# Kernel optimization log

Hardware: AMD Instinct MI355X
Metric: run time of the kernel (lower is better)

The kernel has to match this reference:

```python
import jax, jax.numpy as jnp
import numpy as np

D_MODEL = 1024
N_HEAD = 16


def setup_inputs() -> dict:
    key = jax.random.key(0)
    ks = jax.random.split(key, 9)
    d = D_MODEL
    s = 0.02
    return {
        "x": jax.random.normal(ks[0], (4, 2048, d), dtype=jnp.float32),
        "w_q": jax.random.normal(ks[1], (d, d), dtype=jnp.float32) * s,
        "b_q": jax.random.normal(ks[2], (d,), dtype=jnp.float32) * s,
        "w_k": jax.random.normal(ks[3], (d, d), dtype=jnp.float32) * s,
        "b_k": jax.random.normal(ks[4], (d,), dtype=jnp.float32) * s,
        "w_v": jax.random.normal(ks[5], (d, d), dtype=jnp.float32) * s,
        "b_v": jax.random.normal(ks[6], (d,), dtype=jnp.float32) * s,
        "w_o": jax.random.normal(ks[7], (d, d), dtype=jnp.float32) * s,
        "b_o": jax.random.normal(ks[8], (d,), dtype=jnp.float32) * s,
    }


def reference(x, w_q, b_q, w_k, b_k, w_v, b_v, w_o, b_o):
    B, S, D = x.shape
    H = N_HEAD
    dh = D // H

    def split(t):  # [B,S,D] -> [B,H,S,dh]
        return t.reshape(B, S, H, dh).transpose(0, 2, 1, 3)

    q = split(x @ w_q + b_q)
    k = split(x @ w_k + b_k)
    v = split(x @ w_v + b_v)

    scale = 1.0 / jnp.sqrt(jnp.float32(dh))
    score = jnp.einsum("bhqd,bhkd->bhqk", q, k) * scale
    score = jax.nn.softmax(score, axis=-1)
    out = jnp.einsum("bhqk,bhkd->bhqd", score, v)
    out = out.transpose(0, 2, 1, 3).reshape(B, S, D)
    return out @ w_o + b_o
```

## Files before the change

### kernel.cpp

```cpp
#include <hip/hip_runtime.h>


typedef __bf16 bf16x8 __attribute__((ext_vector_type(8)));
typedef float f32x4 __attribute__((ext_vector_type(4)));
typedef float f32x16 __attribute__((ext_vector_type(16)));
typedef unsigned short u16x8 __attribute__((ext_vector_type(8)));
typedef unsigned u32x4 __attribute__((ext_vector_type(4)));
typedef unsigned u32x2 __attribute__((ext_vector_type(2)));

#define SEQ 2048
#define DM 1024
#define NHEAD 16
#define MTOT 8192
#define QSCALE 0.18033688011112042f

__device__ __forceinline__ unsigned short f2bf(float f) {
  unsigned u = __builtin_bit_cast(unsigned, f);
  u += 0x7fffu + ((u >> 16) & 1u);
  return (unsigned short)(u >> 16);
}

__device__ __forceinline__ unsigned pkbf(float lo, float hi) {
  __bf16 a = (__bf16)lo, b = (__bf16)hi;
  return ((unsigned)__builtin_bit_cast(unsigned short, b) << 16) |
         __builtin_bit_cast(unsigned short, a);
}

__device__ __forceinline__ void async16(const void* g, void* l) {
  __builtin_amdgcn_global_load_lds(
      (const __attribute__((address_space(1))) void*)g,
      (__attribute__((address_space(3))) void*)l, 16, 0, 0);
}

template <bool CX>
__device__ __forceinline__ void exch(unsigned A, unsigned B, unsigned& fr0, unsigned& fr2) {
#if __has_builtin(__builtin_amdgcn_permlane32_swap)
  if constexpr (CX) {
    u32x2 r = __builtin_amdgcn_permlane32_swap(B, A, false, false);
    fr0 = r[1]; fr2 = r[0];
  } else {
    u32x2 r = __builtin_amdgcn_permlane32_swap(A, B, false, false);
    fr0 = r[0]; fr2 = r[1];
  }
#else
  int hi = (threadIdx.x & 63) >> 5;
  unsigned sA = (unsigned)__shfl_xor((int)A, 32);
  unsigned sB = (unsigned)__shfl_xor((int)B, 32);
  fr0 = hi ? sB : A;
  fr2 = hi ? B : sA;
#endif
}

__device__ __forceinline__ float halfsum(float rs) {
#if __has_builtin(__builtin_amdgcn_permlane32_swap)
  unsigned rb = __builtin_bit_cast(unsigned, rs);
  u32x2 rr = __builtin_amdgcn_permlane32_swap(rb, rb, false, false);
  return __builtin_bit_cast(float, rr[0]) + __builtin_bit_cast(float, rr[1]);
#else
  return rs + __shfl_xor(rs, 32);
#endif
}

__global__ __launch_bounds__(256) void k_cvt(const float* __restrict__ x,
                                             unsigned short* __restrict__ xb) {
  size_t i = ((size_t)blockIdx.x * 256 + threadIdx.x) * 8;
  float4 a = *(const float4*)(x + i);
  float4 b = *(const float4*)(x + i + 4);
  u16x8 o;
  o[0] = f2bf(a.x); o[1] = f2bf(a.y); o[2] = f2bf(a.z); o[3] = f2bf(a.w);
  o[4] = f2bf(b.x); o[5] = f2bf(b.y); o[6] = f2bf(b.z); o[7] = f2bf(b.w);
  *(u16x8*)(xb + i) = o;
}

__global__ __launch_bounds__(256) void k_wt(const float* __restrict__ w0, const float* __restrict__ w1,
                                            const float* __restrict__ w2, const float* __restrict__ w3,
                                            unsigned short* __restrict__ t0, unsigned short* __restrict__ t1,
                                            unsigned short* __restrict__ t2, unsigned short* __restrict__ t3) {
  __shared__ float t[64][65];
  int z = blockIdx.z;
  const float* w = z == 0 ? w0 : z == 1 ? w1 : z == 2 ? w2 : w3;
  unsigned short* wt = z == 0 ? t0 : z == 1 ? t1 : z == 2 ? t2 : t3;
  int nt = blockIdx.x, kt = blockIdx.y;
  int tx = threadIdx.x & 63, ty = threadIdx.x >> 6;
  for (int i = 0; i < 16; ++i) {
    int r = i * 4 + ty;
    t[r][tx] = w[(size_t)(kt * 64 + r) * DM + nt * 64 + tx];
  }
  __syncthreads();
  for (int i = 0; i < 16; ++i) {
    int r = i * 4 + ty;
    wt[(size_t)(nt * 64 + r) * DM + kt * 64 + tx] = f2bf(t[tx][r]);
  }
}

__device__ __forceinline__ void gemm_body(const unsigned short* __restrict__ A,
                                          const unsigned short* __restrict__ Bt,
                                          const float* __restrict__ bias,
                                          unsigned short* __restrict__ Cb,
                                          float* __restrict__ Cf, int bm, int bn, float sc) {
  __shared__ __align__(16) unsigned short As[128 * 64];
  __shared__ __align__(16) unsigned short Bs[128 * 64];
  const int K = DM, N = DM;
  int tid = threadIdx.x, w = tid >> 6, l = tid & 63;
  int g = l >> 4, l15 = l & 15;
  int wm = (w >> 1) * 64, wn = (w & 1) * 64;
  f32x4 acc[4][4];
#pragma unroll
  for (int mi = 0; mi < 4; ++mi)
#pragma unroll
    for (int ni = 0; ni < 4; ++ni)
#pragma unroll
      for (int e = 0; e < 4; ++e) acc[mi][ni][e] = 0.f;

  int lr8 = l >> 3, lp = l & 7;
  for (int kt = 0; kt < K / 64; ++kt) {
    __syncthreads();
#pragma unroll
    for (int i = 0; i < 4; ++i) {
      int cs = i * 4 + w;
      int row = cs * 8 + lr8;
      int c = lp ^ lr8;
      async16(A + (size_t)(bm + row) * K + kt * 64 + c * 8, &As[cs * 512]);
      async16(Bt + (size_t)(bn + row) * K + kt * 64 + c * 8, &Bs[cs * 512]);
    }
    __syncthreads();
    bf16x8 af[4][2];
#pragma unroll
    for (int mi = 0; mi < 4; ++mi)
#pragma unroll
      for (int kk = 0; kk < 2; ++kk) {
        int row = wm + mi * 16 + l15;
        af[mi][kk] = *(const bf16x8*)&As[row * 64 + (((kk * 4 + g) ^ (row & 7)) * 8)];
      }
    __builtin_amdgcn_s_setprio(1);
#pragma unroll
    for (int ni = 0; ni < 4; ++ni) {
      int row = wn + ni * 16 + l15;
      bf16x8 b0 = *(const bf16x8*)&Bs[row * 64 + (((0 + g) ^ (row & 7)) * 8)];
      bf16x8 b1 = *(const bf16x8*)&Bs[row * 64 + (((4 + g) ^ (row & 7)) * 8)];
#pragma unroll
      for (int mi = 0; mi < 4; ++mi) {
        acc[mi][ni] = __builtin_amdgcn_mfma_f32_16x16x32_bf16(af[mi][0], b0, acc[mi][ni], 0, 0, 0);
        acc[mi][ni] = __builtin_amdgcn_mfma_f32_16x16x32_bf16(af[mi][1], b1, acc[mi][ni], 0, 0, 0);
      }
    }
    __builtin_amdgcn_s_setprio(0);
  }
  float bv[4];
#pragma unroll
  for (int ni = 0; ni < 4; ++ni) bv[ni] = bias[bn + wn + ni * 16 + l15];
#pragma unroll
  for (int mi = 0; mi < 4; ++mi)
#pragma unroll
    for (int ni = 0; ni < 4; ++ni) {
      int col = bn + wn + ni * 16 + l15;
#pragma unroll
      for (int r = 0; r < 4; ++r) {
        int rowg = bm + wm + mi * 16 + g * 4 + r;
        float v = (acc[mi][ni][r] + bv[ni]) * sc;
        if (Cf) Cf[(size_t)rowg * N + col] = v;
        else    Cb[(size_t)rowg * N + col] = f2bf(v);
      }
    }
}

__global__ __launch_bounds__(256) void k_gemm(const unsigned short* __restrict__ A,
                                              const unsigned short* __restrict__ Bt,
                                              const float* __restrict__ bias,
                                              unsigned short* __restrict__ Cb,
                                              float* __restrict__ Cf) {
  gemm_body(A, Bt, bias, Cb, Cf, blockIdx.y * 128, blockIdx.x * 128, 1.f);
}

__global__ __launch_bounds__(256) void k_gemm_qkv(const unsigned short* __restrict__ A,
                                                  const unsigned short* bt0, const unsigned short* bt1,
                                                  const unsigned short* bt2,
                                                  const float* b0, const float* b1, const float* b2,
                                                  unsigned short* o0, unsigned short* o1,
                                                  unsigned short* o2) {
  int which = blockIdx.x >> 3;
  const unsigned short* Bt = which == 0 ? bt0 : which == 1 ? bt1 : bt2;
  const float* bias = which == 0 ? b0 : which == 1 ? b1 : b2;
  unsigned short* Cb = which == 0 ? o0 : which == 1 ? o1 : o2;
  float sc = which == 0 ? QSCALE : 1.f;
  gemm_body(A, Bt, bias, Cb, nullptr, blockIdx.y * 128, (blockIdx.x & 7) * 128, sc);
}

__global__ __launch_bounds__(256) void k_vt(const unsigned short* __restrict__ V,
                                            unsigned short* __restrict__ Vt) {
  __shared__ __align__(16) unsigned short t[64 * 64];
  int st = blockIdx.x, bh = blockIdx.y;
  int b = bh >> 4, h = bh & 15;
  int tid = threadIdx.x, w = tid >> 6, l = tid & 63;
  for (int i = 0; i < 2; ++i) {
    int cs = i * 4 + w;
    int row = cs * 8 + (l >> 3);
    int c = l & 7;
    async16(V + ((size_t)(b * SEQ + st * 64 + row) * DM + h * 64 + c * 8), &t[cs * 512]);
  }
  __syncthreads();
  for (int p = 0; p < 2; ++p) {
    int d = p * 32 + (tid >> 3);
    int cs = tid & 7;
    u16x8 o;
    for (int j = 0; j < 8; ++j) o[j] = t[(cs * 8 + j) * 64 + d];
    *(u16x8*)(Vt + ((size_t)bh * 64 + d) * SEQ + st * 64 + cs * 8) = o;
  }
}

template <bool CX>
__device__ __forceinline__ void attn_core(const unsigned short* __restrict__ Q,
                                          const unsigned short* __restrict__ Kg,
                                          const unsigned short* __restrict__ Vt,
                                          unsigned short* __restrict__ Og,
                                          unsigned short* smem, int b, int h, int bh, int qt) {
  int tid = threadIdx.x, w = tid >> 6, l = tid & 63;
  int l31 = l & 31, hi = l >> 5, l7 = l & 7;
  int lr8 = l >> 3, lp = l & 7;
  int q0w = qt * 256 + w * 64;
  unsigned short* const ks0 = smem;
  unsigned short* const ks1 = smem + 4096;
  unsigned short* const vs0 = smem + 8192;
  unsigned short* const vs1 = smem + 12288;

  bf16x8 qf[2][4];
#pragma unroll
  for (int qh = 0; qh < 2; ++qh)
#pragma unroll
    for (int c = 0; c < 4; ++c)
      qf[qh][c] = *(const bf16x8*)(Q + (size_t)(b * SEQ + q0w + qh * 32 + l31) * DM +
                                   h * 64 + c * 16 + hi * 8);

  float lrow[2] = {0.f, 0.f};
  f32x16 oacc[2][2];
#pragma unroll
  for (int qh = 0; qh < 2; ++qh)
#pragma unroll
    for (int d = 0; d < 2; ++d)
#pragma unroll
      for (int r = 0; r < 16; ++r) oacc[qh][d][r] = 0.f;

  auto stage = [&](int kt, unsigned short* kdst, unsigned short* vdst) {
#pragma unroll
    for (int i = 0; i < 2; ++i) {
      int cs = i * 4 + w;
      int row = cs * 8 + lr8;
      int c = lp ^ lr8;
      async16(Kg + ((size_t)(b * SEQ + kt * 64 + row) * DM + h * 64 + c * 8), kdst + cs * 512);
      async16(Vt + (((size_t)bh * 64 + row) * SEQ + kt * 64 + c * 8), vdst + cs * 512);
    }
  };

  auto tile = [&](int kt, unsigned short* kc, unsigned short* vc,
                  unsigned short* kn, unsigned short* vn) {
    if (kt + 1 < SEQ / 64) stage(kt + 1, kn, vn);

    f32x16 sacc[2][2];
#pragma unroll
    for (int qh = 0; qh < 2; ++qh)
#pragma unroll
      for (int kh = 0; kh < 2; ++kh)
#pragma unroll
        for (int r = 0; r < 16; ++r) sacc[qh][kh][r] = 0.f;
    __builtin_amdgcn_s_setprio(1);
#pragma unroll
    for (int kh = 0; kh < 2; ++kh) {
      const unsigned short* kb = kc + (kh * 32 + l31) * 64;
#pragma unroll
      for (int c = 0; c < 4; ++c) {
        bf16x8 a = *(const bf16x8*)(kb + (((2 * c + hi) ^ l7) << 3));
        sacc[0][kh] = __builtin_amdgcn_mfma_f32_32x32x16_bf16(a, qf[0][c], sacc[0][kh], 0, 0, 0);
        sacc[1][kh] = __builtin_amdgcn_mfma_f32_32x32x16_bf16(a, qf[1][c], sacc[1][kh], 0, 0, 0);
      }
    }
    __builtin_amdgcn_s_setprio(0);

    bf16x8 pf[2][4];
#pragma unroll
    for (int qh = 0; qh < 2; ++qh) {
      float r0 = 0.f, r1 = 0.f, r2 = 0.f, r3 = 0.f;
#pragma unroll
      for (int kh = 0; kh < 2; ++kh)
#pragma unroll
        for (int e = 0; e < 16; e += 4) {
          float p0 = __builtin_amdgcn_exp2f(sacc[qh][kh][e + 0]);
          float p1 = __builtin_amdgcn_exp2f(sacc[qh][kh][e + 1]);
          float p2 = __builtin_amdgcn_exp2f(sacc[qh][kh][e + 2]);
          float p3 = __builtin_amdgcn_exp2f(sacc[qh][kh][e + 3]);
          sacc[qh][kh][e + 0] = p0; sacc[qh][kh][e + 1] = p1;
          sacc[qh][kh][e + 2] = p2; sacc[qh][kh][e + 3] = p3;
          r0 += p0; r1 += p1; r2 += p2; r3 += p3;
        }
      lrow[qh] += halfsum((r0 + r1) + (r2 + r3));
#pragma unroll
      for (int ks = 0; ks < 4; ++ks) {
        int kh = ks >> 1, q4 = (ks & 1) * 8;
        unsigned A0 = pkbf(sacc[qh][kh][q4 + 0], sacc[qh][kh][q4 + 1]);
        unsigned A1 = pkbf(sacc[qh][kh][q4 + 2], sacc[qh][kh][q4 + 3]);
        unsigned B0 = pkbf(sacc[qh][kh][q4 + 4], sacc[qh][kh][q4 + 5]);
        unsigned B1 = pkbf(sacc[qh][kh][q4 + 6], sacc[qh][kh][q4 + 7]);
        unsigned f0, f1, f2, f3;
        exch<CX>(A0, B0, f0, f2);
        exch<CX>(A1, B1, f1, f3);
        u32x4 fr; fr[0] = f0; fr[1] = f1; fr[2] = f2; fr[3] = f3;
        pf[qh][ks] = __builtin_bit_cast(bf16x8, fr);
      }
    }

    __builtin_amdgcn_s_setprio(1);
#pragma unroll
    for (int d = 0; d < 2; ++d) {
      const unsigned short* vb = vc + (d * 32 + l31) * 64;
#pragma unroll
      for (int ks = 0; ks < 4; ++ks) {
        bf16x8 a = *(const bf16x8*)(vb + (((2 * ks + hi) ^ l7) << 3));
        oacc[0][d] = __builtin_amdgcn_mfma_f32_32x32x16_bf16(a, pf[0][ks], oacc[0][d], 0, 0, 0);
        oacc[1][d] = __builtin_amdgcn_mfma_f32_32x32x16_bf16(a, pf[1][ks], oacc[1][d], 0, 0, 0);
      }
    }
    __builtin_amdgcn_s_setprio(0);
    __syncthreads();
  };

  stage(0, ks0, vs0);
  __syncthreads();
  for (int kt = 0; kt < SEQ / 64; kt += 2) {
    tile(kt, ks0, vs0, ks1, vs1);
    tile(kt + 1, ks1, vs1, ks0, vs0);
  }

  unsigned* ot = (unsigned*)smem + w * (32 * 33);
#pragma unroll
  for (int qh = 0; qh < 2; ++qh) {
    float inv = 1.f / lrow[qh];
#pragma unroll
    for (int d = 0; d < 2; ++d)
#pragma unroll
      for (int qd = 0; qd < 4; ++qd) {
        unsigned u0 = pkbf(oacc[qh][d][qd * 4 + 0] * inv, oacc[qh][d][qd * 4 + 1] * inv);
        unsigned u1 = pkbf(oacc[qh][d][qd * 4 + 2] * inv, oacc[qh][d][qd * 4 + 3] * inv);
        int idx = l31 * 33 + d * 16 + qd * 4 + hi * 2;
        ot[idx] = u0;
        ot[idx + 1] = u1;
      }
    int row = l >> 1, half = l & 1;
    const unsigned* sr = (const unsigned*)smem + w * (32 * 33) + row * 33 + half * 16;
    unsigned o[16];
#pragma unroll
    for (int j = 0; j < 16; ++j) o[j] = sr[j];
    size_t gbase = (size_t)(b * SEQ + q0w + qh * 32 + row) * DM + h * 64 + half * 32;
#pragma unroll
    for (int i = 0; i < 4; ++i) {
      u32x4 t;
      t[0] = o[i * 4 + 0]; t[1] = o[i * 4 + 1]; t[2] = o[i * 4 + 2]; t[3] = o[i * 4 + 3];
      *(u32x4*)(Og + gbase * 1 + i * 8) = t;
    }
  }
}

__global__ __launch_bounds__(256, 2) void k_attn(const unsigned short* __restrict__ Q,
                                                 const unsigned short* __restrict__ Kg,
                                                 const unsigned short* __restrict__ Vt,
                                                 unsigned short* __restrict__ Og) {
  __shared__ __align__(16) unsigned short smem[16384];
  int bh = blockIdx.x, qt = blockIdx.y;
  int b = bh >> 4, h = bh & 15;
#if __has_builtin(__builtin_amdgcn_permlane32_swap)
  unsigned lid = threadIdx.x & 63;
  u32x2 pr = __builtin_amdgcn_permlane32_swap(lid, lid + 64u, false, false);
  bool convX = __builtin_amdgcn_readfirstlane(pr[0]) >= 64u;
#else
  bool convX = false;
#endif
  if (convX) attn_core<true>(Q, Kg, Vt, Og, smem, b, h, bh, qt);
  else       attn_core<false>(Q, Kg, Vt, Og, smem, b, h, bh, qt);
}

extern "C" void kernel_launch(void* const* d_in, const int* in_sizes, int n_in,
                              void* d_out, int out_size, void* d_ws, size_t ws_size,
                              hipStream_t stream) {
  const float* x  = (const float*)d_in[0];
  const float* wq = (const float*)d_in[1];
  const float* bq = (const float*)d_in[2];
  const float* wk = (const float*)d_in[3];
  const float* bk = (const float*)d_in[4];
  const float* wv = (const float*)d_in[5];
  const float* bv = (const float*)d_in[6];
  const float* wo = (const float*)d_in[7];
  const float* bo = (const float*)d_in[8];

  const size_t SZ_X = (size_t)MTOT * DM * 2;
  const size_t SZ_W = (size_t)DM * DM * 2;
  char* ws = (char*)d_ws;
  size_t off = 0;
  unsigned short* xb  = (unsigned short*)(ws + off); off += SZ_X;
  unsigned short* wqT = (unsigned short*)(ws + off); off += SZ_W;
  unsigned short* wkT = (unsigned short*)(ws + off); off += SZ_W;
  unsigned short* wvT = (unsigned short*)(ws + off); off += SZ_W;
  unsigned short* woT = (unsigned short*)(ws + off); off += SZ_W;
  unsigned short* Qb  = (unsigned short*)(ws + off); off += SZ_X;
  unsigned short* Kb  = (unsigned short*)(ws + off); off += SZ_X;
  unsigned short* Vb  = (unsigned short*)(ws + off); off += SZ_X;
  unsigned short* Vtb = (unsigned short*)(ws + off); off += SZ_X;
  unsigned short* Ab  = (unsigned short*)(ws + off); off += SZ_X;
  if (ws_size < off) return;

  k_cvt<<<dim3(4096), dim3(256), 0, stream>>>(x, xb);
  k_wt<<<dim3(16, 16, 4), dim3(256), 0, stream>>>(wq, wk, wv, wo, wqT, wkT, wvT, woT);
  k_gemm_qkv<<<dim3(24, 64), dim3(256), 0, stream>>>(xb, wqT, wkT, wvT, bq, bk, bv, Qb, Kb, Vb);
  k_vt<<<dim3(32, 64), dim3(256), 0, stream>>>(Vb, Vtb);
  k_attn<<<dim3(64, 8), dim3(256), 0, stream>>>(Qb, Kb, Vtb, Ab);
  k_gemm<<<dim3(8, 64), dim3(256), 0, stream>>>(Ab, woT, bo, nullptr, (float*)d_out);
}
```

Measured before the change: 181.2 us.

## Deepen attention K/V prefetch to a 4-slot ring with explicit vmcnt waits

The attention kernel moves from a double-buffered K/V stage with a full __syncthreads per tile to a four-slot LDS ring. Loads are issued two tiles ahead and gated by explicit s_waitcnt vmcnt(4) plus a raw s_barrier, which aims to hide global-to-LDS latency and drop the implicit full waitcnt. LDS per block doubles to 64 KB, which may limit occupancy under launch_bounds(256,2). The first QK MFMA now takes a zero accumulator directly instead of zero-initialising sacc.

Measured after the change: 181.9 us. Within noise of the previous version (+0.4%).

```diff
diff --git a/kernel.cpp b/kernel.cpp
--- a/kernel.cpp
+++ b/kernel.cpp
@@ -218,10 +218,8 @@
   int l31 = l & 31, hi = l >> 5, l7 = l & 7;
   int lr8 = l >> 3, lp = l & 7;
   int q0w = qt * 256 + w * 64;
-  unsigned short* const ks0 = smem;
-  unsigned short* const ks1 = smem + 4096;
-  unsigned short* const vs0 = smem + 8192;
-  unsigned short* const vs1 = smem + 12288;
+  unsigned short* const KS = smem;
+  unsigned short* const VS = smem + 16384;
 
   bf16x8 qf[2][4];
 #pragma unroll
@@ -231,43 +229,43 @@
       qf[qh][c] = *(const bf16x8*)(Q + (size_t)(b * SEQ + q0w + qh * 32 + l31) * DM +
                                    h * 64 + c * 16 + hi * 8);
 
+  const f32x16 fz = {0.f, 0.f, 0.f, 0.f, 0.f, 0.f, 0.f, 0.f,
+                     0.f, 0.f, 0.f, 0.f, 0.f, 0.f, 0.f, 0.f};
   float lrow[2] = {0.f, 0.f};
   f32x16 oacc[2][2];
 #pragma unroll
   for (int qh = 0; qh < 2; ++qh)
 #pragma unroll
-    for (int d = 0; d < 2; ++d)
-#pragma unroll
-      for (int r = 0; r < 16; ++r) oacc[qh][d][r] = 0.f;
-
-  auto stage = [&](int kt, unsigned short* kdst, unsigned short* vdst) {
+    for (int d = 0; d < 2; ++d) oacc[qh][d] = fz;
+
+  auto stage = [&](int kt) {
+    int s = kt & 3;
+    unsigned short* kd = KS + s * 4096;
+    unsigned short* vd = VS + s * 4096;
 #pragma unroll
     for (int i = 0; i < 2; ++i) {
       int cs = i * 4 + w;
       int row = cs * 8 + lr8;
       int c = lp ^ lr8;
-      async16(Kg + ((size_t)(b * SEQ + kt * 64 + row) * DM + h * 64 + c * 8), kdst + cs * 512);
-      async16(Vt + (((size_t)bh * 64 + row) * SEQ + kt * 64 + c * 8), vdst + cs * 512);
+      async16(Kg + ((size_t)(b * SEQ + kt * 64 + row) * DM + h * 64 + c * 8), kd + cs * 512);
+      async16(Vt + (((size_t)bh * 64 + row) * SEQ + kt * 64 + c * 8), vd + cs * 512);
     }
   };
 
-  auto tile = [&](int kt, unsigned short* kc, unsigned short* vc,
-                  unsigned short* kn, unsigned short* vn) {
-    if (kt + 1 < SEQ / 64) stage(kt + 1, kn, vn);
+  auto compute = [&](int kt) {
+    const unsigned short* kc = KS + (kt & 3) * 4096;
+    const unsigned short* vc = VS + (kt & 3) * 4096;
 
     f32x16 sacc[2][2];
-#pragma unroll
-    for (int qh = 0; qh < 2; ++qh)
-#pragma unroll
-      for (int kh = 0; kh < 2; ++kh)
-#pragma unroll
-        for (int r = 0; r < 16; ++r) sacc[qh][kh][r] = 0.f;
     __builtin_amdgcn_s_setprio(1);
 #pragma unroll
     for (int kh = 0; kh < 2; ++kh) {
       const unsigned short* kb = kc + (kh * 32 + l31) * 64;
-#pragma unroll
-      for (int c = 0; c < 4; ++c) {
+      bf16x8 a0 = *(const bf16x8*)(kb + ((hi ^ l7) << 3));
+      sacc[0][kh] = __builtin_amdgcn_mfma_f32_32x32x16_bf16(a0, qf[0][0], fz, 0, 0, 0);
+      sacc[1][kh] = __builtin_amdgcn_mfma_f32_32x32x16_bf16(a0, qf[1][0], fz, 0, 0, 0);
+#pragma unroll
+      for (int c = 1; c < 4; ++c) {
         bf16x8 a = *(const bf16x8*)(kb + (((2 * c + hi) ^ l7) << 3));
         sacc[0][kh] = __builtin_amdgcn_mfma_f32_32x32x16_bf16(a, qf[0][c], sacc[0][kh], 0, 0, 0);
         sacc[1][kh] = __builtin_amdgcn_mfma_f32_32x32x16_bf16(a, qf[1][c], sacc[1][kh], 0, 0, 0);
@@ -319,15 +317,34 @@
       }
     }
     __builtin_amdgcn_s_setprio(0);
-    __syncthreads();
   };
 
-  stage(0, ks0, vs0);
-  __syncthreads();
-  for (int kt = 0; kt < SEQ / 64; kt += 2) {
-    tile(kt, ks0, vs0, ks1, vs1);
-    tile(kt + 1, ks1, vs1, ks0, vs0);
-  }
+#define VWAIT4 asm volatile("s_waitcnt vmcnt(4)" ::: "memory")
+#define VWAIT0 asm volatile("s_waitcnt vmcnt(0)" ::: "memory")
+#define BARR                         \
+  __builtin_amdgcn_s_barrier();      \
+  __builtin_amdgcn_sched_barrier(0)
+
+  stage(0);
+  stage(1);
+  VWAIT4;
+  BARR;
+  const int NT = SEQ / 64;
+  for (int kt = 0; kt < NT - 2; ++kt) {
+    stage(kt + 2);
+    compute(kt);
+    VWAIT4;
+    BARR;
+  }
+  compute(NT - 2);
+  VWAIT0;
+  BARR;
+  compute(NT - 1);
+  BARR;
+
+#undef VWAIT4
+#undef VWAIT0
+#undef BARR
 
   unsigned* ot = (unsigned*)smem + w * (32 * 33);
 #pragma unroll
@@ -353,7 +370,7 @@
     for (int i = 0; i < 4; ++i) {
       u32x4 t;
       t[0] = o[i * 4 + 0]; t[1] = o[i * 4 + 1]; t[2] = o[i * 4 + 2]; t[3] = o[i * 4 + 3];
-      *(u32x4*)(Og + gbase * 1 + i * 8) = t;
+      *(u32x4*)(Og + gbase + i * 8) = t;
     }
   }
 }
@@ -362,7 +379,7 @@
                                                  const unsigned short* __restrict__ Kg,
                                                  const unsigned short* __restrict__ Vt,
                                                  unsigned short* __restrict__ Og) {
-  __shared__ __align__(16) unsigned short smem[16384];
+  __shared__ __align__(16) unsigned short smem[32768];
   int bh = blockIdx.x, qt = blockIdx.y;
   int b = bh >> 4, h = bh & 15;
 #if __has_builtin(__builtin_amdgcn_permlane32_swap)
```

## Load K/V fragments directly from global into registers, swizzle GEMM block order

Applied to the files above, without the earlier changes.

The attention kernel no longer stages K and V tiles through shared memory with async copies and barriers. Each wave now loads its own 32-key K and V fragments straight from global memory into registers, double-buffered across chunks, and processes 32 keys per step instead of 64. This drops the per-tile __syncthreads and shrinks LDS to the output transpose buffer, at the cost of each wave redundantly fetching K/V from global/L2 instead of sharing it across the four waves. Separately, both GEMM kernels remap block indices so consecutive blocks are spread across rows, aiming for better cache locality.

New measurement: 221.0 us. 22.0% more time.

```diff
diff --git a/kernel.cpp b/kernel.cpp
--- a/kernel.cpp
+++ b/kernel.cpp
@@ -169,7 +169,10 @@
                                               const float* __restrict__ bias,
                                               unsigned short* __restrict__ Cb,
                                               float* __restrict__ Cf) {
-  gemm_body(A, Bt, bias, Cb, Cf, blockIdx.y * 128, blockIdx.x * 128, 1.f);
+  int L = blockIdx.x + blockIdx.y * 8;
+  int Lp = (L & 7) * 64 + (L >> 3);
+  int bx = Lp & 7, by = Lp >> 3;
+  gemm_body(A, Bt, bias, Cb, Cf, by * 128, bx * 128, 1.f);
 }
 
 __global__ __launch_bounds__(256) void k_gemm_qkv(const unsigned short* __restrict__ A,
@@ -178,12 +181,15 @@
                                                   const float* b0, const float* b1, const float* b2,
                                                   unsigned short* o0, unsigned short* o1,
                                                   unsigned short* o2) {
-  int which = blockIdx.x >> 3;
+  int L = blockIdx.x + blockIdx.y * 24;
+  int Lp = (L & 7) * 192 + (L >> 3);
+  int bx = Lp % 24, by = Lp / 24;
+  int which = bx >> 3;
   const unsigned short* Bt = which == 0 ? bt0 : which == 1 ? bt1 : bt2;
   const float* bias = which == 0 ? b0 : which == 1 ? b1 : b2;
   unsigned short* Cb = which == 0 ? o0 : which == 1 ? o1 : o2;
   float sc = which == 0 ? QSCALE : 1.f;
-  gemm_body(A, Bt, bias, Cb, nullptr, blockIdx.y * 128, (blockIdx.x & 7) * 128, sc);
+  gemm_body(A, Bt, bias, Cb, nullptr, by * 128, (bx & 7) * 128, sc);
 }
 
 __global__ __launch_bounds__(256) void k_vt(const unsigned short* __restrict__ V,
@@ -213,92 +219,76 @@
                                           const unsigned short* __restrict__ Kg,
                                           const unsigned short* __restrict__ Vt,
                                           unsigned short* __restrict__ Og,
-                                          unsigned short* smem, int b, int h, int bh, int qt) {
+                                          unsigned* smem, int b, int h, int bh, int qt) {
   int tid = threadIdx.x, w = tid >> 6, l = tid & 63;
-  int l31 = l & 31, hi = l >> 5, l7 = l & 7;
-  int lr8 = l >> 3, lp = l & 7;
+  int l31 = l & 31, hi = l >> 5;
   int q0w = qt * 256 + w * 64;
-  unsigned short* const ks0 = smem;
-  unsigned short* const ks1 = smem + 4096;
-  unsigned short* const vs0 = smem + 8192;
-  unsigned short* const vs1 = smem + 12288;
 
   bf16x8 qf[2][4];
 #pragma unroll
   for (int qh = 0; qh < 2; ++qh)
 #pragma unroll
-    for (int c = 0; c < 4; ++c)
-      qf[qh][c] = *(const bf16x8*)(Q + (size_t)(b * SEQ + q0w + qh * 32 + l31) * DM +
-                                   h * 64 + c * 16 + hi * 8);
-
+    for (int j = 0; j < 4; ++j)
+      qf[qh][j] = *(const bf16x8*)(Q + (size_t)(b * SEQ + q0w + qh * 32 + l31) * DM +
+                                   h * 64 + j * 16 + hi * 8);
+
+  const f32x16 fz = {0.f, 0.f, 0.f, 0.f, 0.f, 0.f, 0.f, 0.f,
+                     0.f, 0.f, 0.f, 0.f, 0.f, 0.f, 0.f, 0.f};
   float lrow[2] = {0.f, 0.f};
   f32x16 oacc[2][2];
 #pragma unroll
   for (int qh = 0; qh < 2; ++qh)
 #pragma unroll
-    for (int d = 0; d < 2; ++d)
-#pragma unroll
-      for (int r = 0; r < 16; ++r) oacc[qh][d][r] = 0.f;
-
-  auto stage = [&](int kt, unsigned short* kdst, unsigned short* vdst) {
-#pragma unroll
-    for (int i = 0; i < 2; ++i) {
-      int cs = i * 4 + w;
-      int row = cs * 8 + lr8;
-      int c = lp ^ lr8;
-      async16(Kg + ((size_t)(b * SEQ + kt * 64 + row) * DM + h * 64 + c * 8), kdst + cs * 512);
-      async16(Vt + (((size_t)bh * 64 + row) * SEQ + kt * 64 + c * 8), vdst + cs * 512);
-    }
+    for (int d = 0; d < 2; ++d) oacc[qh][d] = fz;
+
+  const unsigned short* kbase = Kg + ((size_t)(b * SEQ + l31) * DM) + h * 64 + hi * 8;
+  const unsigned short* vbase = Vt + (((size_t)bh * 64 + l31) * SEQ) + hi * 8;
+
+  auto loadKV = [&](int c, bf16x8 (&kf)[4], bf16x8 (&vf)[4]) {
+    const unsigned short* kp = kbase + (size_t)c * 32 * DM;
+#pragma unroll
+    for (int j = 0; j < 4; ++j) kf[j] = *(const bf16x8*)(kp + j * 16);
+    const unsigned short* vp = vbase + c * 32;
+    vf[0] = *(const bf16x8*)(vp);
+    vf[1] = *(const bf16x8*)(vp + 16);
+    vf[2] = *(const bf16x8*)(vp + (size_t)32 * SEQ);
+    vf[3] = *(const bf16x8*)(vp + (size_t)32 * SEQ + 16);
   };
 
-  auto tile = [&](int kt, unsigned short* kc, unsigned short* vc,
-                  unsigned short* kn, unsigned short* vn) {
-    if (kt + 1 < SEQ / 64) stage(kt + 1, kn, vn);
-
-    f32x16 sacc[2][2];
-#pragma unroll
-    for (int qh = 0; qh < 2; ++qh)
-#pragma unroll
-      for (int kh = 0; kh < 2; ++kh)
-#pragma unroll
-        for (int r = 0; r < 16; ++r) sacc[qh][kh][r] = 0.f;
+  auto chunk = [&](const bf16x8 (&kf)[4], const bf16x8 (&vf)[4]) {
+    f32x16 sacc[2];
     __builtin_amdgcn_s_setprio(1);
-#pragma unroll
-    for (int kh = 0; kh < 2; ++kh) {
-      const unsigned short* kb = kc + (kh * 32 + l31) * 64;
-#pragma unroll
-      for (int c = 0; c < 4; ++c) {
-        bf16x8 a = *(const bf16x8*)(kb + (((2 * c + hi) ^ l7) << 3));
-        sacc[0][kh] = __builtin_amdgcn_mfma_f32_32x32x16_bf16(a, qf[0][c], sacc[0][kh], 0, 0, 0);
-        sacc[1][kh] = __builtin_amdgcn_mfma_f32_32x32x16_bf16(a, qf[1][c], sacc[1][kh], 0, 0, 0);
-      }
+    sacc[0] = __builtin_amdgcn_mfma_f32_32x32x16_bf16(kf[0], qf[0][0], fz, 0, 0, 0);
+    sacc[1] = __builtin_amdgcn_mfma_f32_32x32x16_bf16(kf[0], qf[1][0], fz, 0, 0, 0);
+#pragma unroll
+    for (int j = 1; j < 4; ++j) {
+      sacc[0] = __builtin_amdgcn_mfma_f32_32x32x16_bf16(kf[j], qf[0][j], sacc[0], 0, 0, 0);
+      sacc[1] = __builtin_amdgcn_mfma_f32_32x32x16_bf16(kf[j], qf[1][j], sacc[1], 0, 0, 0);
     }
     __builtin_amdgcn_s_setprio(0);
 
-    bf16x8 pf[2][4];
+    bf16x8 pf[2][2];
 #pragma unroll
     for (int qh = 0; qh < 2; ++qh) {
       float r0 = 0.f, r1 = 0.f, r2 = 0.f, r3 = 0.f;
 #pragma unroll
-      for (int kh = 0; kh < 2; ++kh)
-#pragma unroll
-        for (int e = 0; e < 16; e += 4) {
-          float p0 = __builtin_amdgcn_exp2f(sacc[qh][kh][e + 0]);
-          float p1 = __builtin_amdgcn_exp2f(sacc[qh][kh][e + 1]);
-          float p2 = __builtin_amdgcn_exp2f(sacc[qh][kh][e + 2]);
-          float p3 = __builtin_amdgcn_exp2f(sacc[qh][kh][e + 3]);
-          sacc[qh][kh][e + 0] = p0; sacc[qh][kh][e + 1] = p1;
-          sacc[qh][kh][e + 2] = p2; sacc[qh][kh][e + 3] = p3;
-          r0 += p0; r1 += p1; r2 += p2; r3 += p3;
-        }
+      for (int e = 0; e < 16; e += 4) {
+        float p0 = __builtin_amdgcn_exp2f(sacc[qh][e + 0]);
+        float p1 = __builtin_amdgcn_exp2f(sacc[qh][e + 1]);
+        float p2 = __builtin_amdgcn_exp2f(sacc[qh][e + 2]);
+        float p3 = __builtin_amdgcn_exp2f(sacc[qh][e + 3]);
+        sacc[qh][e + 0] = p0; sacc[qh][e + 1] = p1;
+        sacc[qh][e + 2] = p2; sacc[qh][e + 3] = p3;
+        r0 += p0; r1 += p1; r2 += p2; r3 += p3;
+      }
       lrow[qh] += halfsum((r0 + r1) + (r2 + r3));
 #pragma unroll
-      for (int ks = 0; ks < 4; ++ks) {
-        int kh = ks >> 1, q4 = (ks & 1) * 8;
-        unsigned A0 = pkbf(sacc[qh][kh][q4 + 0], sacc[qh][kh][q4 + 1]);
-        unsigned A1 = pkbf(sacc[qh][kh][q4 + 2], sacc[qh][kh][q4 + 3]);
-        unsigned B0 = pkbf(sacc[qh][kh][q4 + 4], sacc[qh][kh][q4 + 5]);
-        unsigned B1 = pkbf(sacc[qh][kh][q4 + 6], sacc[qh][kh][q4 + 7]);
+      for (int ks = 0; ks < 2; ++ks) {
+        int q4 = ks * 8;
+        unsigned A0 = pkbf(sacc[qh][q4 + 0], sacc[qh][q4 + 1]);
+        unsigned A1 = pkbf(sacc[qh][q4 + 2], sacc[qh][q4 + 3]);
+        unsigned B0 = pkbf(sacc[qh][q4 + 4], sacc[qh][q4 + 5]);
+        unsigned B1 = pkbf(sacc[qh][q4 + 6], sacc[qh][q4 + 7]);
         unsigned f0, f1, f2, f3;
         exch<CX>(A0, B0, f0, f2);
         exch<CX>(A1, B1, f1, f3);
@@ -309,27 +299,26 @@
 
     __builtin_amdgcn_s_setprio(1);
 #pragma unroll
-    for (int d = 0; d < 2; ++d) {
-      const unsigned short* vb = vc + (d * 32 + l31) * 64;
-#pragma unroll
-      for (int ks = 0; ks < 4; ++ks) {
-        bf16x8 a = *(const bf16x8*)(vb + (((2 * ks + hi) ^ l7) << 3));
-        oacc[0][d] = __builtin_amdgcn_mfma_f32_32x32x16_bf16(a, pf[0][ks], oacc[0][d], 0, 0, 0);
-        oacc[1][d] = __builtin_amdgcn_mfma_f32_32x32x16_bf16(a, pf[1][ks], oacc[1][d], 0, 0, 0);
-      }
-    }
+    for (int d = 0; d < 2; ++d)
+#pragma unroll
+      for (int ks = 0; ks < 2; ++ks) {
+        oacc[0][d] = __builtin_amdgcn_mfma_f32_32x32x16_bf16(vf[d * 2 + ks], pf[0][ks], oacc[0][d], 0, 0, 0);
+        oacc[1][d] = __builtin_amdgcn_mfma_f32_32x32x16_bf16(vf[d * 2 + ks], pf[1][ks], oacc[1][d], 0, 0, 0);
+      }
     __builtin_amdgcn_s_setprio(0);
-    __syncthreads();
   };
 
-  stage(0, ks0, vs0);
-  __syncthreads();
-  for (int kt = 0; kt < SEQ / 64; kt += 2) {
-    tile(kt, ks0, vs0, ks1, vs1);
-    tile(kt + 1, ks1, vs1, ks0, vs0);
-  }
-
-  unsigned* ot = (unsigned*)smem + w * (32 * 33);
+  const int NC = SEQ / 32;
+  bf16x8 kfA[4], vfA[4], kfB[4], vfB[4];
+  loadKV(0, kfA, vfA);
+  for (int c = 0; c < NC; c += 2) {
+    loadKV(c + 1, kfB, vfB);
+    chunk(kfA, vfA);
+    if (c + 2 < NC) loadKV(c + 2, kfA, vfA);
+    chunk(kfB, vfB);
+  }
+
+  unsigned* ot = smem + w * (32 * 33);
 #pragma unroll
   for (int qh = 0; qh < 2; ++qh) {
     float inv = 1.f / lrow[qh];
@@ -344,7 +333,7 @@
         ot[idx + 1] = u1;
       }
     int row = l >> 1, half = l & 1;
-    const unsigned* sr = (const unsigned*)smem + w * (32 * 33) + row * 33 + half * 16;
+    const unsigned* sr = ot + row * 33 + half * 16;
     unsigned o[16];
 #pragma unroll
     for (int j = 0; j < 16; ++j) o[j] = sr[j];
@@ -353,7 +342,7 @@
     for (int i = 0; i < 4; ++i) {
       u32x4 t;
       t[0] = o[i * 4 + 0]; t[1] = o[i * 4 + 1]; t[2] = o[i * 4 + 2]; t[3] = o[i * 4 + 3];
-      *(u32x4*)(Og + gbase * 1 + i * 8) = t;
+      *(u32x4*)(Og + gbase + i * 8) = t;
     }
   }
 }
@@ -362,7 +351,7 @@
                                                  const unsigned short* __restrict__ Kg,
                                                  const unsigned short* __restrict__ Vt,
                                                  unsigned short* __restrict__ Og) {
-  __shared__ __align__(16) unsigned short smem[16384];
+  __shared__ __align__(16) unsigned smem[4 * 32 * 33];
   int bh = blockIdx.x, qt = blockIdx.y;
   int b = bh >> 4, h = bh & 15;
 #if __has_builtin(__builtin_amdgcn_permlane32_swap)
```

## Split attention KV range across two wave groups and swizzle GEMM block order

Applied to the files above, without the earlier changes.

The attention kernel now launches 512 threads per block. Two sets of four waves each process half of the key/value sequence for the same query tile, with their own double-buffered LDS. The partial output accumulators and row sums are then combined through shared memory before normalization. This shortens the serial KV loop per wave and raises in-flight work, at the cost of doubled LDS, an extra reduction step and lower block occupancy. Separately, both GEMM kernels remap block indices so that consecutively scheduled blocks are spread across row tiles, to change cache locality across CUs/XCDs.

Result: slower. 542.0 us (+199.1%).

```diff
diff --git a/kernel.cpp b/kernel.cpp
--- a/kernel.cpp
+++ b/kernel.cpp
@@ -169,7 +169,10 @@
                                               const float* __restrict__ bias,
                                               unsigned short* __restrict__ Cb,
                                               float* __restrict__ Cf) {
-  gemm_body(A, Bt, bias, Cb, Cf, blockIdx.y * 128, blockIdx.x * 128, 1.f);
+  int L = blockIdx.x + blockIdx.y * 8;
+  int Lp = (L & 7) * 64 + (L >> 3);
+  int bx = Lp & 7, by = Lp >> 3;
+  gemm_body(A, Bt, bias, Cb, Cf, by * 128, bx * 128, 1.f);
 }
 
 __global__ __launch_bounds__(256) void k_gemm_qkv(const unsigned short* __restrict__ A,
@@ -178,12 +181,15 @@
                                                   const float* b0, const float* b1, const float* b2,
                                                   unsigned short* o0, unsigned short* o1,
                                                   unsigned short* o2) {
-  int which = blockIdx.x >> 3;
+  int L = blockIdx.x + blockIdx.y * 24;
+  int Lp = (L & 7) * 192 + (L >> 3);
+  int bx = Lp % 24, by = Lp / 24;
+  int which = bx >> 3;
   const unsigned short* Bt = which == 0 ? bt0 : which == 1 ? bt1 : bt2;
   const float* bias = which == 0 ? b0 : which == 1 ? b1 : b2;
   unsigned short* Cb = which == 0 ? o0 : which == 1 ? o1 : o2;
   float sc = which == 0 ? QSCALE : 1.f;
-  gemm_body(A, Bt, bias, Cb, nullptr, blockIdx.y * 128, (blockIdx.x & 7) * 128, sc);
+  gemm_body(A, Bt, bias, Cb, nullptr, by * 128, (bx & 7) * 128, sc);
 }
 
 __global__ __launch_bounds__(256) void k_vt(const unsigned short* __restrict__ V,
@@ -215,13 +221,12 @@
                                           unsigned short* __restrict__ Og,
                                           unsigned short* smem, int b, int h, int bh, int qt) {
   int tid = threadIdx.x, w = tid >> 6, l = tid & 63;
+  int kvset = w >> 2, wq = w & 3;
   int l31 = l & 31, hi = l >> 5, l7 = l & 7;
   int lr8 = l >> 3, lp = l & 7;
-  int q0w = qt * 256 + w * 64;
-  unsigned short* const ks0 = smem;
-  unsigned short* const ks1 = smem + 4096;
-  unsigned short* const vs0 = smem + 8192;
-  unsigned short* const vs1 = smem + 12288;
+  int q0w = qt * 256 + wq * 64;
+  int kvrow0 = kvset * 1024;
+  unsigned short* const SB = smem + kvset * 16384;
 
   bf16x8 qf[2][4];
 #pragma unroll
@@ -231,43 +236,50 @@
       qf[qh][c] = *(const bf16x8*)(Q + (size_t)(b * SEQ + q0w + qh * 32 + l31) * DM +
                                    h * 64 + c * 16 + hi * 8);
 
+  const f32x16 fz = {0.f, 0.f, 0.f, 0.f, 0.f, 0.f, 0.f, 0.f,
+                     0.f, 0.f, 0.f, 0.f, 0.f, 0.f, 0.f, 0.f};
   float lrow[2] = {0.f, 0.f};
   f32x16 oacc[2][2];
 #pragma unroll
   for (int qh = 0; qh < 2; ++qh)
 #pragma unroll
-    for (int d = 0; d < 2; ++d)
-#pragma unroll
-      for (int r = 0; r < 16; ++r) oacc[qh][d][r] = 0.f;
-
-  auto stage = [&](int kt, unsigned short* kdst, unsigned short* vdst) {
+    for (int d = 0; d < 2; ++d) oacc[qh][d] = fz;
+
+  auto stage = [&](int kt) {
+    int s = kt & 1;
+    unsigned short* kd = SB + s * 8192;
+    unsigned short* vd = kd + 4096;
 #pragma unroll
     for (int i = 0; i < 2; ++i) {
-      int cs = i * 4 + w;
+      int cs = i * 4 + wq;
       int row = cs * 8 + lr8;
       int c = lp ^ lr8;
-      async16(Kg + ((size_t)(b * SEQ + kt * 64 + row) * DM + h * 64 + c * 8), kdst + cs * 512);
-      async16(Vt + (((size_t)bh * 64 + row) * SEQ + kt * 64 + c * 8), vdst + cs * 512);
+      async16(Kg + ((size_t)(b * SEQ + kvrow0 + kt * 64 + row) * DM + h * 64 + c * 8),
+              kd + cs * 512);
+      async16(Vt + (((size_t)bh * 64 + row) * SEQ + kvrow0 + kt * 64 + c * 8),
+              vd + cs * 512);
     }
   };
 
-  auto tile = [&](int kt, unsigned short* kc, unsigned short* vc,
-                  unsigned short* kn, unsigned short* vn) {
-    if (kt + 1 < SEQ / 64) stage(kt + 1, kn, vn);
+  const int NT = 1024 / 64;
+  stage(0);
+  __syncthreads();
+  for (int t = 0; t < NT; ++t) {
+    int cur = t & 1;
+    if (t + 1 < NT) stage(t + 1);
+    const unsigned short* kc = SB + cur * 8192;
+    const unsigned short* vc = kc + 4096;
 
     f32x16 sacc[2][2];
-#pragma unroll
-    for (int qh = 0; qh < 2; ++qh)
-#pragma unroll
-      for (int kh = 0; kh < 2; ++kh)
-#pragma unroll
-        for (int r = 0; r < 16; ++r) sacc[qh][kh][r] = 0.f;
     __builtin_amdgcn_s_setprio(1);
 #pragma unroll
     for (int kh = 0; kh < 2; ++kh) {
       const unsigned short* kb = kc + (kh * 32 + l31) * 64;
-#pragma unroll
-      for (int c = 0; c < 4; ++c) {
+      bf16x8 a0 = *(const bf16x8*)(kb + ((hi ^ l7) << 3));
+      sacc[0][kh] = __builtin_amdgcn_mfma_f32_32x32x16_bf16(a0, qf[0][0], fz, 0, 0, 0);
+      sacc[1][kh] = __builtin_amdgcn_mfma_f32_32x32x16_bf16(a0, qf[1][0], fz, 0, 0, 0);
+#pragma unroll
+      for (int c = 1; c < 4; ++c) {
         bf16x8 a = *(const bf16x8*)(kb + (((2 * c + hi) ^ l7) << 3));
         sacc[0][kh] = __builtin_amdgcn_mfma_f32_32x32x16_bf16(a, qf[0][c], sacc[0][kh], 0, 0, 0);
         sacc[1][kh] = __builtin_amdgcn_mfma_f32_32x32x16_bf16(a, qf[1][c], sacc[1][kh], 0, 0, 0);
@@ -320,49 +332,80 @@
     }
     __builtin_amdgcn_s_setprio(0);
     __syncthreads();
-  };
-
-  stage(0, ks0, vs0);
+  }
+
+  float* part = (float*)smem;
+  float* lr = (float*)(smem + 32768);
+  if (kvset == 1) {
+    float* base = part + wq * 4096 + l * 4;
+#pragma unroll
+    for (int qh = 0; qh < 2; ++qh) {
+#pragma unroll
+      for (int d = 0; d < 2; ++d)
+#pragma unroll
+        for (int r4 = 0; r4 < 4; ++r4) {
+          f32x4 v;
+          v[0] = oacc[qh][d][r4 * 4 + 0]; v[1] = oacc[qh][d][r4 * 4 + 1];
+          v[2] = oacc[qh][d][r4 * 4 + 2]; v[3] = oacc[qh][d][r4 * 4 + 3];
+          *(f32x4*)(base + ((qh * 2 + d) * 4 + r4) * 256) = v;
+        }
+      lr[(wq * 2 + qh) * 64 + l] = lrow[qh];
+    }
+  }
   __syncthreads();
-  for (int kt = 0; kt < SEQ / 64; kt += 2) {
-    tile(kt, ks0, vs0, ks1, vs1);
-    tile(kt + 1, ks1, vs1, ks0, vs0);
-  }
-
-  unsigned* ot = (unsigned*)smem + w * (32 * 33);
-#pragma unroll
-  for (int qh = 0; qh < 2; ++qh) {
-    float inv = 1.f / lrow[qh];
-#pragma unroll
-    for (int d = 0; d < 2; ++d)
-#pragma unroll
-      for (int qd = 0; qd < 4; ++qd) {
-        unsigned u0 = pkbf(oacc[qh][d][qd * 4 + 0] * inv, oacc[qh][d][qd * 4 + 1] * inv);
-        unsigned u1 = pkbf(oacc[qh][d][qd * 4 + 2] * inv, oacc[qh][d][qd * 4 + 3] * inv);
-        int idx = l31 * 33 + d * 16 + qd * 4 + hi * 2;
-        ot[idx] = u0;
-        ot[idx + 1] = u1;
-      }
-    int row = l >> 1, half = l & 1;
-    const unsigned* sr = (const unsigned*)smem + w * (32 * 33) + row * 33 + half * 16;
-    unsigned o[16];
-#pragma unroll
-    for (int j = 0; j < 16; ++j) o[j] = sr[j];
-    size_t gbase = (size_t)(b * SEQ + q0w + qh * 32 + row) * DM + h * 64 + half * 32;
-#pragma unroll
-    for (int i = 0; i < 4; ++i) {
-      u32x4 t;
-      t[0] = o[i * 4 + 0]; t[1] = o[i * 4 + 1]; t[2] = o[i * 4 + 2]; t[3] = o[i * 4 + 3];
-      *(u32x4*)(Og + gbase * 1 + i * 8) = t;
-    }
-  }
-}
-
-__global__ __launch_bounds__(256, 2) void k_attn(const unsigned short* __restrict__ Q,
+  if (kvset == 0) {
+    float* base = part + wq * 4096 + l * 4;
+#pragma unroll
+    for (int qh = 0; qh < 2; ++qh) {
+#pragma unroll
+      for (int d = 0; d < 2; ++d)
+#pragma unroll
+        for (int r4 = 0; r4 < 4; ++r4) {
+          f32x4 v = *(const f32x4*)(base + ((qh * 2 + d) * 4 + r4) * 256);
+          oacc[qh][d][r4 * 4 + 0] += v[0]; oacc[qh][d][r4 * 4 + 1] += v[1];
+          oacc[qh][d][r4 * 4 + 2] += v[2]; oacc[qh][d][r4 * 4 + 3] += v[3];
+        }
+      lrow[qh] += lr[(wq * 2 + qh) * 64 + l];
+    }
+  }
+  __syncthreads();
+
+  if (kvset == 0) {
+    unsigned* ot = (unsigned*)smem + wq * (32 * 33);
+#pragma unroll
+    for (int qh = 0; qh < 2; ++qh) {
+      float inv = 1.f / lrow[qh];
+#pragma unroll
+      for (int d = 0; d < 2; ++d)
+#pragma unroll
+        for (int qd = 0; qd < 4; ++qd) {
+          unsigned u0 = pkbf(oacc[qh][d][qd * 4 + 0] * inv, oacc[qh][d][qd * 4 + 1] * inv);
+          unsigned u1 = pkbf(oacc[qh][d][qd * 4 + 2] * inv, oacc[qh][d][qd * 4 + 3] * inv);
+          int idx = l31 * 33 + d * 16 + qd * 4 + hi * 2;
+          ot[idx] = u0;
+          ot[idx + 1] = u1;
+        }
+      int row = l >> 1, half = l & 1;
+      const unsigned* sr = (const unsigned*)smem + wq * (32 * 33) + row * 33 + half * 16;
+      unsigned o[16];
+#pragma unroll
+      for (int j = 0; j < 16; ++j) o[j] = sr[j];
+      size_t gbase = (size_t)(b * SEQ + q0w + qh * 32 + row) * DM + h * 64 + half * 32;
+#pragma unroll
+      for (int i = 0; i < 4; ++i) {
+        u32x4 t;
+        t[0] = o[i * 4 + 0]; t[1] = o[i * 4 + 1]; t[2] = o[i * 4 + 2]; t[3] = o[i * 4 + 3];
+        *(u32x4*)(Og + gbase + i * 8) = t;
+      }
+    }
+  }
+}
+
+__global__ __launch_bounds__(512, 4) void k_attn(const unsigned short* __restrict__ Q,
                                                  const unsigned short* __restrict__ Kg,
                                                  const unsigned short* __restrict__ Vt,
                                                  unsigned short* __restrict__ Og) {
-  __shared__ __align__(16) unsigned short smem[16384];
+  __shared__ __align__(16) unsigned short smem[33792];
   int bh = blockIdx.x, qt = blockIdx.y;
   int b = bh >> 4, h = bh & 15;
 #if __has_builtin(__builtin_amdgcn_permlane32_swap)
@@ -409,6 +452,6 @@
   k_wt<<<dim3(16, 16, 4), dim3(256), 0, stream>>>(wq, wk, wv, wo, wqT, wkT, wvT, woT);
   k_gemm_qkv<<<dim3(24, 64), dim3(256), 0, stream>>>(xb, wqT, wkT, wvT, bq, bk, bv, Qb, Kb, Vb);
   k_vt<<<dim3(32, 64), dim3(256), 0, stream>>>(Vb, Vtb);
-  k_attn<<<dim3(64, 8), dim3(256), 0, stream>>>(Qb, Kb, Vtb, Ab);
+  k_attn<<<dim3(64, 8), dim3(512), 0, stream>>>(Qb, Kb, Vtb, Ab);
   k_gemm<<<dim3(8, 64), dim3(256), 0, stream>>>(Ab, woT, bo, nullptr, (float*)d_out);
 }
```
